# Optimization experiments

Measured on AMD Instinct MI355X. Metric: run time of the kernel, lower is better.

Reference implementation:

```python
import jax, jax.numpy as jnp
import numpy as np


def setup_inputs() -> dict:
    key = jax.random.key(0)
    vel = jax.random.normal(key, (10000, 1000, 3), dtype=jnp.float32)
    return {"vel": vel, "vacf_window": 100}


def reference(vel, vacf_window):
    # vel: [T, N, 3]; output: [vacf_window]
    T = vel.shape[0]
    flat = vel.reshape(T, -1)  # [T, N*3]
    # lag 0: mean(vel * vel)
    terms = [jnp.mean(flat * flat)]
    # lags 1..vacf_window-1: mean over (T - t) * N * 3 elements
    for t in range(1, vacf_window):
        terms.append(jnp.mean(flat[t:] * flat[:-t]))
    return jnp.stack(terms)
```

## Files before the change

kernel.cpp:

```cpp
#include <hip/hip_runtime.h>


#define T_DIM 10000
#define C_DIM 3000
#define W 100
#define MA 256
#define NA 16
#define SROWS 384
#define NBB 40
#define KS 96
#define KW 32
#define SPX 12
#define NPART 32

typedef __attribute__((ext_vector_type(8))) short short8;
typedef __attribute__((ext_vector_type(4))) short short4v;
typedef __attribute__((ext_vector_type(4))) float float4v;

__device__ __forceinline__ short f2bf(float f) {
    unsigned u = __float_as_uint(f);
    u += 0x7fffu + ((u >> 16) & 1u);
    return (short)(u >> 16);
}

__global__ __launch_bounds__(256, 3)
void vacf_fused(const float* __restrict__ X, float* __restrict__ partial) {
    const int tid  = threadIdx.x;
    const int lane = tid & 63;
    const int wv   = tid >> 6;
    const int xcd  = blockIdx.x & 7;
    const int u    = blockIdx.x >> 3;
    const int ksix = xcd + 8 * (u / NBB);
    const int bb   = u % NBB;
    const int i0   = bb * MA;
    const int c0   = ksix * KW;

    __shared__ __align__(16) char lds[SROWS * 64];
    __shared__ float bins[W];
    if (tid < W) bins[tid] = 0.f;

    const int rr = tid >> 3;
    const int cl = (tid & 7) * 4;
    const int sw = ((((cl >> 3) ^ ((rr >> 1) & 3)) << 4) | ((cl & 7) << 1));

    const bool fast = (i0 + SROWS <= T_DIM) && (c0 + KW <= C_DIM);
    if (fast) {
        float4v v[12];
        #pragma unroll
        for (int m = 0; m < 12; ++m)
            v[m] = *(const float4v*)(X + (size_t)(i0 + m * 32 + rr) * C_DIM + c0 + cl);
        #pragma unroll
        for (int m = 0; m < 12; ++m) {
            short4v o;
            o[0] = f2bf(v[m][0]); o[1] = f2bf(v[m][1]);
            o[2] = f2bf(v[m][2]); o[3] = f2bf(v[m][3]);
            *(short4v*)&lds[(m * 32 + rr) * 64 + sw] = o;
        }
    } else {
        #pragma unroll
        for (int m = 0; m < 12; ++m) {
            const int row = m * 32 + rr;
            const int gr  = i0 + row;
            float4v v = {0.f, 0.f, 0.f, 0.f};
            if (gr < T_DIM && c0 + cl + 4 <= C_DIM)
                v = *(const float4v*)(X + (size_t)gr * C_DIM + c0 + cl);
            short4v o;
            o[0] = f2bf(v[0]); o[1] = f2bf(v[1]);
            o[2] = f2bf(v[2]); o[3] = f2bf(v[3]);
            *(short4v*)&lds[row * 64 + sw] = o;
        }
    }
    __syncthreads();

    const int n    = lane & 15;
    const int quad = lane >> 4;
    const int d0   = 2 * wv;

    float4v acc0 = {0.f, 0.f, 0.f, 0.f};
    float4v acc1 = {0.f, 0.f, 0.f, 0.f};

    const char* lb = lds + n * 64 + ((quad ^ ((n >> 1) & 3)) << 4);
    short8 fbp = *(const short8*)(lb + d0 * 1024);
    #pragma unroll
    for (int a = 0; a < NA; ++a) {
        const short8 fav = *(const short8*)(lb + a * 1024);
        const short8 fbn = *(const short8*)(lb + (d0 + a + 1) * 1024);
        acc0 = __builtin_amdgcn_mfma_f32_16x16x32_bf16(fav, fbp, acc0, 0, 0, 0);
        acc1 = __builtin_amdgcn_mfma_f32_16x16x32_bf16(fav, fbn, acc1, 0, 0, 0);
        fbp = fbn;
    }

    #pragma unroll
    for (int p = 0; p < 4; ++p) {
        const int m  = quad * 4 + p;
        const int t0 = 16 * d0 + n - m;
        if (t0 >= 0 && t0 < W) atomicAdd(&bins[t0], acc0[p]);
        const int t1 = t0 + 16;
        if (t1 >= 0 && t1 < W) atomicAdd(&bins[t1], acc1[p]);
    }
    __syncthreads();
    if (tid < W) atomicAdd(&partial[(blockIdx.x & (NPART - 1)) * W + tid], bins[tid]);
}

__global__ void vacf_scale(const float* __restrict__ partial, float* __restrict__ out) {
    int t = threadIdx.x;
    if (t < W) {
        float s = 0.f;
        #pragma unroll
        for (int b = 0; b < NPART; ++b) s += partial[b * W + t];
        out[t] = s / ((float)(T_DIM - t) * (float)C_DIM);
    }
}

extern "C" void kernel_launch(void* const* d_in, const int* in_sizes, int n_in,
                              void* d_out, int out_size, void* d_ws, size_t ws_size,
                              hipStream_t stream) {
    const float* X = (const float*)d_in[0];
    float* out = (float*)d_out;
    float* ws  = (float*)d_ws;

    hipMemsetAsync(ws, 0, NPART * W * sizeof(float), stream);
    vacf_fused<<<KS * NBB, 256, 0, stream>>>(X, ws);
    vacf_scale<<<1, 128, 0, stream>>>(ws, out);
}
```

Baseline: 188.4 us.

## Make VACF kernel persistent with double-buffered LDS tile prefetch

Replaces the one-tile-per-block launch with a fixed grid of 768 blocks. Each block loops over tiles, loading the next tile's global data into registers while running the MFMAs on the current LDS buffer, then writing it into the other buffer. The aim is to hide global load latency behind compute and to cut block launch and epilogue overhead. The column tile count also drops from 96 to 94 so no blocks cover only padding, and the partial-sum slots go from 32 to 8. In exchange the block uses twice the LDS, the explicit XCD-aware tile mapping is gone, and blocks end up with uneven numbers of tiles.

```diff
diff --git a/kernel.cpp b/kernel.cpp
--- a/kernel.cpp
+++ b/kernel.cpp
@@ -8,10 +8,12 @@
 #define NA 16
 #define SROWS 384
 #define NBB 40
-#define KS 96
+#define KS 94
 #define KW 32
-#define SPX 12
-#define NPART 32
+#define NT (KS * NBB)
+#define GRID 768
+#define TILE_B (SROWS * 64)
+#define NPART 8
 
 typedef __attribute__((ext_vector_type(8))) short short8;
 typedef __attribute__((ext_vector_type(4))) short short4v;
@@ -23,19 +25,47 @@
     return (short)(u >> 16);
 }
 
+__device__ __forceinline__ void load_tile(const float* __restrict__ X, int t,
+                                          int rr, int cl, float4v* v) {
+    const int bb   = t / KS;
+    const int ksix = t - bb * KS;
+    const int i0   = bb * MA;
+    const int c0   = ksix * KW;
+    if ((i0 + SROWS <= T_DIM) & (c0 + KW <= C_DIM)) {
+        const float* p = X + (size_t)(i0 + rr) * C_DIM + c0 + cl;
+        #pragma unroll
+        for (int m = 0; m < 12; ++m)
+            v[m] = *(const float4v*)(p + (size_t)(m * 32) * C_DIM);
+    } else {
+        #pragma unroll
+        for (int m = 0; m < 12; ++m) {
+            const int gr = i0 + m * 32 + rr;
+            float4v z = {0.f, 0.f, 0.f, 0.f};
+            if (gr < T_DIM && c0 + cl + 4 <= C_DIM)
+                z = *(const float4v*)(X + (size_t)gr * C_DIM + c0 + cl);
+            v[m] = z;
+        }
+    }
+}
+
+__device__ __forceinline__ void store_tile(char* __restrict__ buf,
+                                           int rr, int sw, const float4v* v) {
+    #pragma unroll
+    for (int m = 0; m < 12; ++m) {
+        short4v o;
+        o[0] = f2bf(v[m][0]); o[1] = f2bf(v[m][1]);
+        o[2] = f2bf(v[m][2]); o[3] = f2bf(v[m][3]);
+        *(short4v*)&buf[(m * 32 + rr) * 64 + sw] = o;
+    }
+}
+
 __global__ __launch_bounds__(256, 3)
 void vacf_fused(const float* __restrict__ X, float* __restrict__ partial) {
     const int tid  = threadIdx.x;
     const int lane = tid & 63;
     const int wv   = tid >> 6;
-    const int xcd  = blockIdx.x & 7;
-    const int u    = blockIdx.x >> 3;
-    const int ksix = xcd + 8 * (u / NBB);
-    const int bb   = u % NBB;
-    const int i0   = bb * MA;
-    const int c0   = ksix * KW;
 
-    __shared__ __align__(16) char lds[SROWS * 64];
+    __shared__ __align__(16) char lds[2 * TILE_B];
     __shared__ float bins[W];
     if (tid < W) bins[tid] = 0.f;
 
@@ -43,51 +73,46 @@
     const int cl = (tid & 7) * 4;
     const int sw = ((((cl >> 3) ^ ((rr >> 1) & 3)) << 4) | ((cl & 7) << 1));
 
-    const bool fast = (i0 + SROWS <= T_DIM) && (c0 + KW <= C_DIM);
-    if (fast) {
-        float4v v[12];
-        #pragma unroll
-        for (int m = 0; m < 12; ++m)
-            v[m] = *(const float4v*)(X + (size_t)(i0 + m * 32 + rr) * C_DIM + c0 + cl);
-        #pragma unroll
-        for (int m = 0; m < 12; ++m) {
-            short4v o;
-            o[0] = f2bf(v[m][0]); o[1] = f2bf(v[m][1]);
-            o[2] = f2bf(v[m][2]); o[3] = f2bf(v[m][3]);
-            *(short4v*)&lds[(m * 32 + rr) * 64 + sw] = o;
-        }
-    } else {
-        #pragma unroll
-        for (int m = 0; m < 12; ++m) {
-            const int row = m * 32 + rr;
-            const int gr  = i0 + row;
-            float4v v = {0.f, 0.f, 0.f, 0.f};
-            if (gr < T_DIM && c0 + cl + 4 <= C_DIM)
-                v = *(const float4v*)(X + (size_t)gr * C_DIM + c0 + cl);
-            short4v o;
-            o[0] = f2bf(v[0]); o[1] = f2bf(v[1]);
-            o[2] = f2bf(v[2]); o[3] = f2bf(v[3]);
-            *(short4v*)&lds[row * 64 + sw] = o;
-        }
-    }
-    __syncthreads();
-
     const int n    = lane & 15;
     const int quad = lane >> 4;
     const int d0   = 2 * wv;
+    const int fragoff = n * 64 + ((quad ^ ((n >> 1) & 3)) << 4);
 
     float4v acc0 = {0.f, 0.f, 0.f, 0.f};
     float4v acc1 = {0.f, 0.f, 0.f, 0.f};
+    float4v v[12];
 
-    const char* lb = lds + n * 64 + ((quad ^ ((n >> 1) & 3)) << 4);
-    short8 fbp = *(const short8*)(lb + d0 * 1024);
-    #pragma unroll
-    for (int a = 0; a < NA; ++a) {
-        const short8 fav = *(const short8*)(lb + a * 1024);
-        const short8 fbn = *(const short8*)(lb + (d0 + a + 1) * 1024);
-        acc0 = __builtin_amdgcn_mfma_f32_16x16x32_bf16(fav, fbp, acc0, 0, 0, 0);
-        acc1 = __builtin_amdgcn_mfma_f32_16x16x32_bf16(fav, fbn, acc1, 0, 0, 0);
-        fbp = fbn;
+    int t = blockIdx.x;
+    load_tile(X, t, rr, cl, v);
+    store_tile(lds, rr, sw, v);
+    __syncthreads();
+
+    int cur = 0;
+    while (true) {
+        const int tn = t + GRID;
+        const bool more = (tn < NT);
+        if (more) load_tile(X, tn, rr, cl, v);
+        __builtin_amdgcn_sched_barrier(0);
+
+        {
+            const char* lb = lds + cur * TILE_B + fragoff;
+            short8 fbp = *(const short8*)(lb + d0 * 1024);
+            #pragma unroll
+            for (int a = 0; a < NA; ++a) {
+                const short8 fav = *(const short8*)(lb + a * 1024);
+                const short8 fbn = *(const short8*)(lb + (d0 + a + 1) * 1024);
+                acc0 = __builtin_amdgcn_mfma_f32_16x16x32_bf16(fav, fbp, acc0, 0, 0, 0);
+                acc1 = __builtin_amdgcn_mfma_f32_16x16x32_bf16(fav, fbn, acc1, 0, 0, 0);
+                fbp = fbn;
+            }
+        }
+        __builtin_amdgcn_sched_barrier(0);
+
+        if (more) store_tile(lds + (cur ^ 1) * TILE_B, rr, sw, v);
+        __syncthreads();
+        if (!more) break;
+        cur ^= 1;
+        t = tn;
     }
 
     #pragma unroll
@@ -120,6 +145,6 @@
     float* ws  = (float*)d_ws;
 
     hipMemsetAsync(ws, 0, NPART * W * sizeof(float), stream);
-    vacf_fused<<<KS * NBB, 256, 0, stream>>>(X, ws);
+    vacf_fused<<<GRID, 256, 0, stream>>>(X, ws);
     vacf_scale<<<1, 128, 0, stream>>>(ws, out);
 }
```

Result: faster. 184.5 us (-2.1%).
